# Kernel tuning notes

Hardware: AMD Instinct MI355X
Metric: run time of the kernel (lower is better)

The kernel has to match this reference:

```python
import jax, jax.numpy as jnp
import numpy as np

R = 2  # upscale factor (init kwarg r)

def setup_inputs() -> dict:
    key = jax.random.key(0)
    x = jax.random.normal(key, (32, 256, 256, 12), dtype=jnp.float32)
    return {"x": x}

def reference(x) -> jnp.ndarray:
    # Faithful translation of Subpixel._phase_shift:
    # out[n, i*r + r2, j*r + r1, q] = x[n, i, j, q*r*r + r1*r + r2]
    B, a, b, c = x.shape
    r = R
    q = c // (r * r)
    X = x.reshape(B, a, b, q, r, r)          # (B, a, b, q, r1, r2)
    X = X.transpose(0, 1, 5, 2, 4, 3)        # (B, a, r2, b, r1, q)
    return X.reshape(B, a * r, b * r, q)     # (B, a*r, b*r, q)
```

## Files before the change

kernel.cpp:

```cpp
#include <hip/hip_runtime.h>
#include <hip/hip_bf16.h>


#define B  32
#define H  256
#define W  256
#define C  12
#define Q  3
#define OW (W * 2)

__global__ __launch_bounds__(256) void subpixel_kernel(const float* __restrict__ x,
                                                       float* __restrict__ out) {
    const int idx = blockIdx.x * blockDim.x + threadIdx.x;
    const int j = idx & (W - 1);
    const int i = (idx >> 8) & (H - 1);
    const int n = idx >> 16;

    const float4* __restrict__ inp = reinterpret_cast<const float4*>(x + (size_t)idx * C);
    const float4 v0 = inp[0];
    const float4 v1 = inp[1];
    const float4 v2 = inp[2];

    float* __restrict__ o0 = out + ((size_t)((n * (H * 2) + 2 * i) * OW + 2 * j)) * Q;
    float* __restrict__ o1 = o0 + (size_t)OW * Q;

    float2* __restrict__ s0 = reinterpret_cast<float2*>(o0);
    float2* __restrict__ s1 = reinterpret_cast<float2*>(o1);
    s0[0] = make_float2(v0.x, v1.x);
    s0[1] = make_float2(v2.x, v0.z);
    s0[2] = make_float2(v1.z, v2.z);
    s1[0] = make_float2(v0.y, v1.y);
    s1[1] = make_float2(v2.y, v0.w);
    s1[2] = make_float2(v1.w, v2.w);
}

extern "C" void kernel_launch(void* const* d_in, const int* in_sizes, int n_in,
                              void* d_out, int out_size, void* d_ws, size_t ws_size,
                              hipStream_t stream) {
    const float* x = (const float*)d_in[0];
    float* out = (float*)d_out;

    const int n_pix = B * H * W;
    const int block = 256;
    const int grid = n_pix / block;
    subpixel_kernel<<<grid, block, 0, stream>>>(x, out);
}
```

Baseline: 35.51 us.

## Stage each input row through LDS to emit fully coalesced float4 stores

Each block now handles one input row of 256 pixels (3072 floats). It loads the row with coalesced float4 reads, scatters the values into shared memory in output order (two output rows), then writes them back with contiguous float4 stores. This replaces the strided float2 global stores of the old per-pixel mapping, which wrote through partially used cache lines. The cost is a shared-memory round trip, a barrier and possible LDS bank conflicts on the scatter.

```diff
diff --git a/kernel.cpp b/kernel.cpp
--- a/kernel.cpp
+++ b/kernel.cpp
@@ -5,33 +5,39 @@
 #define B  32
 #define H  256
 #define W  256
-#define C  12
-#define Q  3
-#define OW (W * 2)
+
+typedef float f4 __attribute__((ext_vector_type(4)));
 
 __global__ __launch_bounds__(256) void subpixel_kernel(const float* __restrict__ x,
                                                        float* __restrict__ out) {
-    const int idx = blockIdx.x * blockDim.x + threadIdx.x;
-    const int j = idx & (W - 1);
-    const int i = (idx >> 8) & (H - 1);
-    const int n = idx >> 16;
+    __shared__ float lds[3072];
 
-    const float4* __restrict__ inp = reinterpret_cast<const float4*>(x + (size_t)idx * C);
-    const float4 v0 = inp[0];
-    const float4 v1 = inp[1];
-    const float4 v2 = inp[2];
+    const int blk = blockIdx.x;
+    const int t   = threadIdx.x;
 
-    float* __restrict__ o0 = out + ((size_t)((n * (H * 2) + 2 * i) * OW + 2 * j)) * Q;
-    float* __restrict__ o1 = o0 + (size_t)OW * Q;
+    const f4* __restrict__ rowin  = reinterpret_cast<const f4*>(x   + (size_t)blk * 3072);
+    f4* __restrict__       rowout = reinterpret_cast<f4*>      (out + (size_t)blk * 3072);
 
-    float2* __restrict__ s0 = reinterpret_cast<float2*>(o0);
-    float2* __restrict__ s1 = reinterpret_cast<float2*>(o1);
-    s0[0] = make_float2(v0.x, v1.x);
-    s0[1] = make_float2(v2.x, v0.z);
-    s0[2] = make_float2(v1.z, v2.z);
-    s1[0] = make_float2(v0.y, v1.y);
-    s1[1] = make_float2(v2.y, v0.w);
-    s1[2] = make_float2(v1.w, v2.w);
+#pragma unroll
+    for (int k = 0; k < 3; ++k) {
+        const int u = t + k * 256;
+        const f4 v = rowin[u];
+        const int p = u / 3;
+        const int q = u - 3 * p;
+        const int b = 6 * p + q;
+        lds[b]        = v.x;
+        lds[b + 1536] = v.y;
+        lds[b + 3]    = v.z;
+        lds[b + 1539] = v.w;
+    }
+    __syncthreads();
+
+    const f4* __restrict__ lds4 = reinterpret_cast<const f4*>(lds);
+#pragma unroll
+    for (int k = 0; k < 3; ++k) {
+        const int u = t + k * 256;
+        rowout[u] = lds4[u];
+    }
 }
 
 extern "C" void kernel_launch(void* const* d_in, const int* in_sizes, int n_in,
@@ -40,8 +46,6 @@
     const float* x = (const float*)d_in[0];
     float* out = (float*)d_out;
 
-    const int n_pix = B * H * W;
-    const int block = 256;
-    const int grid = n_pix / block;
-    subpixel_kernel<<<grid, block, 0, stream>>>(x, out);
+    const int grid = B * H;
+    subpixel_kernel<<<grid, 256, 0, stream>>>(x, out);
 }
```

New measurement: 34.70 us. 2.3% less time.
